# Kernel optimization log

Hardware: AMD Instinct MI355X
Metric: run time of the kernel (lower is better)

The kernel has to match this reference:

```python
import jax, jax.numpy as jnp
import numpy as np

# Norse LIFParameters defaults (method='super', alpha=100)
DT = 1e-3
TAU_SYN_INV = 200.0   # 1 / 5e-3
TAU_MEM_INV = 100.0   # 1 / 1e-2
V_TH = 1.0
V_LEAK = 0.0
V_RESET = 0.0
ALPHA = 100.0

@jax.custom_vjp
def superspike(x):
    return (x > 0).astype(x.dtype)

def _ss_fwd(x):
    return superspike(x), x

def _ss_bwd(x, g):
    return (g / (ALPHA * jnp.abs(x) + 1.0) ** 2,)

superspike.defvjp(_ss_fwd, _ss_bwd)

T, B, F, H1, OUT = 100, 512, 784, 1024, 10

def setup_inputs() -> dict:
    key = jax.random.key(0)
    k1, k2, k3 = jax.random.split(key, 3)
    x = jax.random.normal(k1, (T, B, F), jnp.float32)
    # fc0: Linear(784, h1) with bias
    W0 = jax.random.normal(k2, (H1, F), jnp.float32) / np.sqrt(F)
    b0 = jnp.zeros((H1,), jnp.float32)
    # LILinearCell input_weights: Linear(h1, 10) without bias
    Wout = jax.random.normal(k3, (OUT, H1), jnp.float32) / np.sqrt(H1)
    return {"x": x, "W0": W0, "b0": b0, "Wout": Wout}

def reference(x, W0, b0, Wout):
    Tn, Bn, Fn = x.shape
    H = W0.shape[0]
    O = Wout.shape[0]

    def step(state, xt):
        v_lif, i_lif, v_li, i_li = state
        z_in = xt @ W0.T + b0                                    # [B, H]
        # LIF cell step
        v_dec = v_lif + DT * TAU_MEM_INV * ((V_LEAK - v_lif) + i_lif)
        i_dec = i_lif * (1.0 - DT * TAU_SYN_INV)
        z = superspike(v_dec - V_TH)                             # spikes [B, H]
        v_new = (1.0 - z) * v_dec + z * V_RESET
        i_new = i_dec + z_in
        # LI linear cell step (voltage output)
        v_li_new = v_li + DT * TAU_MEM_INV * ((V_LEAK - v_li) + i_li)
        i_li_new = i_li * (1.0 - DT * TAU_SYN_INV) + z @ Wout.T  # [B, O]
        return (v_new, i_new, v_li_new, i_li_new), v_li_new

    z0 = lambda s: jnp.zeros(s, x.dtype)
    init = (z0((Bn, H)), z0((Bn, H)), z0((Bn, O)), z0((Bn, O)))
    _, voltages = jax.lax.scan(step, init, x)
    return voltages  # [T, B, 10]
```

## Files before the change

### kernel.cpp

```cpp
#include <hip/hip_runtime.h>

#define T_TOT 100
#define BATCH 512
#define FIN   784
#define HID   1024
#define NOUT  10
#define KP    800
#define BK    32
#define KSTEPS 25
#define NGRP  16

#define A_HI 0
#define A_LO 8192
#define B_HI 16384
#define B_LO 24576

typedef _Float16 f16x8 __attribute__((ext_vector_type(8)));
typedef float    f32x4 __attribute__((ext_vector_type(4)));

#define AS1C(p) ((const __attribute__((address_space(1))) void*)(p))
#define AS3(p)  ((__attribute__((address_space(3))) void*)(p))

__global__ __launch_bounds__(256)
void cvt_split(const float* __restrict__ src, _Float16* __restrict__ hi,
               _Float16* __restrict__ lo, int nrows)
{
    int idx = blockIdx.x * 256 + threadIdx.x;
    if (idx >= nrows * 100) return;
    int row = idx / 100;
    int k0  = (idx - row * 100) * 8;
    f16x8 h, l;
    if (k0 < FIN) {
        float4 a = *(const float4*)(src + (size_t)row * FIN + k0);
        float4 b = *(const float4*)(src + (size_t)row * FIN + k0 + 4);
        float xs[8] = {a.x, a.y, a.z, a.w, b.x, b.y, b.z, b.w};
        #pragma unroll
        for (int j = 0; j < 8; ++j) {
            _Float16 hh = (_Float16)xs[j];
            h[j] = hh;
            l[j] = (_Float16)((xs[j] - (float)hh) * 4096.0f);
        }
    } else {
        #pragma unroll
        for (int j = 0; j < 8; ++j) { h[j] = (_Float16)0.f; l[j] = (_Float16)0.f; }
    }
    *(f16x8*)(hi + (size_t)row * KP + k0) = h;
    *(f16x8*)(lo + (size_t)row * KP + k0) = l;
}

__global__ __launch_bounds__(256, 2)
void gemm_fused(const float* __restrict__ X,
                const _Float16* __restrict__ Whi, const _Float16* __restrict__ Wlo,
                const float* __restrict__ bias, float* __restrict__ Z, int mb)
{
    __shared__ char smem[65536];
    const int tid  = threadIdx.x;
    const int lane = tid & 63;
    const int wid  = tid >> 6;
    const int wm   = wid >> 1;
    const int wn   = wid & 1;
    const int fr   = lane & 15;
    const int fg   = lane >> 4;

    const int j = blockIdx.x;
    int bm, bn;
    if ((mb & 7) == 0) {
        bm = (j & 7) | ((j >> 6) << 3);
        bn = (j >> 3) & 7;
    } else {
        bm = j >> 3;
        bn = j & 7;
    }
    const size_t row0 = (size_t)bm * 128;
    const int    col0 = bn * 128;

    f32x4 accm[4][4], accc[4][4];
    #pragma unroll
    for (int a = 0; a < 4; ++a)
        #pragma unroll
        for (int b = 0; b < 4; ++b) {
            accm[a][b] = (f32x4){0.f, 0.f, 0.f, 0.f};
            accc[a][b] = (f32x4){0.f, 0.f, 0.f, 0.f};
        }

    const int arow  = tid >> 1;
    const int ahalf = tid & 1;
    float4 ar[4];
    auto aload = [&](int kt) {
        const int kof = kt * BK + ahalf * 16;
        const float* src = X + (row0 + arow) * (size_t)FIN + kof;
        #pragma unroll
        for (int c = 0; c < 4; ++c)
            ar[c] = (kof + c * 4 < FIN) ? *(const float4*)(src + c * 4)
                                        : make_float4(0.f, 0.f, 0.f, 0.f);
    };
    auto cvtwrite = [&](int buf) {
        char* base = smem + buf * 32768;
        #pragma unroll
        for (int cc = 0; cc < 2; ++cc) {
            float xs[8];
            *(float4*)&xs[0] = ar[cc * 2];
            *(float4*)&xs[4] = ar[cc * 2 + 1];
            f16x8 h, l;
            #pragma unroll
            for (int e = 0; e < 8; ++e) {
                _Float16 hh = (_Float16)xs[e];
                h[e] = hh;
                l[e] = (_Float16)((xs[e] - (float)hh) * 4096.0f);
            }
            const int ch  = ahalf * 2 + cc;
            const int chs = ch ^ ((arow >> 1) & 3);
            const int off = arow * 64 + chs * 16;
            *(f16x8*)(base + A_HI + off) = h;
            *(f16x8*)(base + A_LO + off) = l;
        }
    };
    auto stageB = [&](int buf, int kt) {
        const int kof = kt * BK;
        #pragma unroll
        for (int q = 0; q < 2; ++q) {
            const int lin = q * 256 + tid;
            const int row = lin >> 2;
            const int pos = lin & 3;
            const int gg  = pos ^ ((row >> 1) & 3);
            const int ldsw = buf * 32768 + q * 4096 + wid * 1024;
            const size_t gb = (size_t)(col0 + row) * KP + kof + gg * 8;
            __builtin_amdgcn_global_load_lds(AS1C(Whi + gb), AS3(smem + ldsw + B_HI), 16, 0, 0);
            __builtin_amdgcn_global_load_lds(AS1C(Wlo + gb), AS3(smem + ldsw + B_LO), 16, 0, 0);
        }
    };

    auto compute = [&](int buf) {
        const char* base = smem + buf * 32768;
        f16x8 ah[4], al[4], bh[4], bl[4];
        #pragma unroll
        for (int mf = 0; mf < 4; ++mf) {
            const int row = wm * 64 + mf * 16 + fr;
            const int off = row * 64 + ((fg ^ ((row >> 1) & 3)) << 4);
            ah[mf] = *(const f16x8*)(base + A_HI + off);
            al[mf] = *(const f16x8*)(base + A_LO + off);
        }
        #pragma unroll
        for (int nf = 0; nf < 4; ++nf) {
            const int row = wn * 64 + nf * 16 + fr;
            const int off = row * 64 + ((fg ^ ((row >> 1) & 3)) << 4);
            bh[nf] = *(const f16x8*)(base + B_HI + off);
            bl[nf] = *(const f16x8*)(base + B_LO + off);
        }
        #pragma unroll
        for (int mf = 0; mf < 4; ++mf)
            #pragma unroll
            for (int nf = 0; nf < 4; ++nf) {
                accm[mf][nf] = __builtin_amdgcn_mfma_f32_16x16x32_f16(ah[mf], bh[nf], accm[mf][nf], 0, 0, 0);
                accc[mf][nf] = __builtin_amdgcn_mfma_f32_16x16x32_f16(ah[mf], bl[nf], accc[mf][nf], 0, 0, 0);
                accc[mf][nf] = __builtin_amdgcn_mfma_f32_16x16x32_f16(al[mf], bh[nf], accc[mf][nf], 0, 0, 0);
            }
    };

    aload(0);
    stageB(0, 0);
    cvtwrite(0);

    int buf = 0;
    for (int kt = 0; kt < KSTEPS; ++kt) {
        __syncthreads();
        if (kt + 1 < KSTEPS) {
            aload(kt + 1);
            stageB(buf ^ 1, kt + 1);
        }
        compute(buf);
        if (kt + 1 < KSTEPS) cvtwrite(buf ^ 1);
        buf ^= 1;
    }

    #pragma unroll
    for (int nf = 0; nf < 4; ++nf) {
        const int colg = col0 + wn * 64 + nf * 16 + fr;
        const float bv = bias[colg];
        #pragma unroll
        for (int mf = 0; mf < 4; ++mf) {
            const size_t rowg = row0 + wm * 64 + mf * 16 + fg * 4;
            #pragma unroll
            for (int i = 0; i < 4; ++i)
                Z[(rowg + i) * HID + colg] =
                    accm[mf][nf][i] + accc[mf][nf][i] * 2.44140625e-4f + bv;
        }
    }
}

__device__ __forceinline__ float dpp_sum16(float v)
{
    int x;
    x = __builtin_amdgcn_update_dpp(0, __builtin_bit_cast(int, v), 0xB1, 0xF, 0xF, true);
    v += __builtin_bit_cast(float, x);
    x = __builtin_amdgcn_update_dpp(0, __builtin_bit_cast(int, v), 0x4E, 0xF, 0xF, true);
    v += __builtin_bit_cast(float, x);
    x = __builtin_amdgcn_update_dpp(0, __builtin_bit_cast(int, v), 0x141, 0xF, 0xF, true);
    v += __builtin_bit_cast(float, x);
    x = __builtin_amdgcn_update_dpp(0, __builtin_bit_cast(int, v), 0x140, 0xF, 0xF, true);
    v += __builtin_bit_cast(float, x);
    return v;
}

__global__ __launch_bounds__(256, 2)
void lif_scan(const float* __restrict__ Z, const float* __restrict__ Wout,
              float* __restrict__ S,
              float* __restrict__ st_v, float* __restrict__ st_i,
              int tn, int first, int last)
{
#pragma clang fp contract(off)
    const int tid   = threadIdx.x;
    const int b     = blockIdx.x;
    const int lane  = tid & 63;
    const int w     = tid >> 6;
    const int hglob = w * 256 + lane * 4;

    float wreg[NOUT][4];
    #pragma unroll
    for (int o = 0; o < NOUT; ++o) {
        float4 t4 = *(const float4*)&Wout[o * HID + hglob];
        wreg[o][0] = t4.x; wreg[o][1] = t4.y; wreg[o][2] = t4.z; wreg[o][3] = t4.w;
    }

    float v[4], cu[4];
    if (first) {
        #pragma unroll
        for (int jj = 0; jj < 4; ++jj) { v[jj] = 0.f; cu[jj] = 0.f; }
    } else {
        float4 tv = *(const float4*)&st_v[(size_t)b * HID + hglob];
        float4 ti = *(const float4*)&st_i[(size_t)b * HID + hglob];
        v[0]=tv.x; v[1]=tv.y; v[2]=tv.z; v[3]=tv.w;
        cu[0]=ti.x; cu[1]=ti.y; cu[2]=ti.z; cu[3]=ti.w;
    }

    const float*  Zb    = Z + (size_t)b * HID + hglob;
    const size_t  ZSTEP = (size_t)BATCH * HID;
    const int     g     = w * 4 + (lane >> 4);

    float4 ring[8];
    #pragma unroll
    for (int u = 0; u < 8; ++u)
        ring[u] = (u < tn) ? *(const float4*)(Zb + (size_t)u * ZSTEP)
                           : make_float4(0.f, 0.f, 0.f, 0.f);

    for (int tb = 0; tb < tn; tb += 8) {
        #pragma unroll
        for (int u = 0; u < 8; ++u) {
            const int t = tb + u;
            if (t >= tn) break;
            float4 zc = ring[u];
            if (t + 8 < tn)
                ring[u] = *(const float4*)(Zb + (size_t)(t + 8) * ZSTEP);

            const float za[4] = {zc.x, zc.y, zc.z, zc.w};
            float zf[4];
            bool anyz = false;
            #pragma unroll
            for (int jj = 0; jj < 4; ++jj) {
                float tmp  = (0.0f - v[jj]) + cu[jj];
                float vdec = v[jj] + 0.1f * tmp;
                bool  z    = vdec > 1.0f;
                zf[jj] = z ? 1.0f : 0.0f;
                anyz   = anyz || z;
                v[jj]  = z ? 0.0f : vdec;
                cu[jj] = cu[jj] * 0.8f + za[jj];
            }

            float p[NOUT];
            #pragma unroll
            for (int o = 0; o < NOUT; ++o) p[o] = 0.f;

            if (__any(anyz)) {
                if (anyz) {
                    #pragma unroll
                    for (int o = 0; o < NOUT; ++o)
                        p[o] = zf[0]*wreg[o][0] + zf[1]*wreg[o][1]
                             + zf[2]*wreg[o][2] + zf[3]*wreg[o][3];
                }
                #pragma unroll
                for (int o = 0; o < NOUT; ++o) p[o] = dpp_sum16(p[o]);
            }

            if ((lane & 15) == 0) {
                float* sp = S + ((size_t)t * BATCH + b) * (NGRP * NOUT) + g * NOUT;
                #pragma unroll
                for (int o = 0; o < NOUT; ++o) sp[o] = p[o];
            }
        }
    }

    if (!last) {
        *(float4*)&st_v[(size_t)b * HID + hglob] = make_float4(v[0], v[1], v[2], v[3]);
        *(float4*)&st_i[(size_t)b * HID + hglob] = make_float4(cu[0], cu[1], cu[2], cu[3]);
    }
}

__global__ __launch_bounds__(256)
void li_scan(const float* __restrict__ S, float* __restrict__ out,
             float* __restrict__ st_vli, float* __restrict__ st_ili,
             int t0, int tn, int first, int last)
{
#pragma clang fp contract(off)
    const int team = blockIdx.x * 16 + (threadIdx.x >> 4);
    const int g    = threadIdx.x & 15;
    const int b    = team / NOUT;
    const int o    = team - b * NOUT;

    float vli = 0.f, ili = 0.f;
    if (!first) { vli = st_vli[team]; ili = st_ili[team]; }

    const float* Sp   = S + ((size_t)b * NGRP + g) * NOUT + o;
    const size_t STEP = (size_t)BATCH * NGRP * NOUT;

    float rg[4];
    #pragma unroll
    for (int u = 0; u < 4; ++u)
        rg[u] = (u < tn) ? Sp[(size_t)u * STEP] : 0.f;

    for (int tb = 0; tb < tn; tb += 4) {
        #pragma unroll
        for (int u = 0; u < 4; ++u) {
            const int t = tb + u;
            if (t >= tn) break;
            float val = rg[u];
            if (t + 4 < tn) rg[u] = Sp[(size_t)(t + 4) * STEP];
            float s = dpp_sum16(val);
            float tmp  = (0.0f - vli) + ili;
            float vnew = vli + 0.1f * tmp;
            ili = ili * 0.8f + s;
            vli = vnew;
            if (g == 0)
                out[((size_t)(t0 + t) * BATCH + b) * NOUT + o] = vnew;
        }
    }
    if (!last && g == 0) { st_vli[team] = vli; st_ili[team] = ili; }
}

extern "C" void kernel_launch(void* const* d_in, const int* in_sizes, int n_in,
                              void* d_out, int out_size, void* d_ws, size_t ws_size,
                              hipStream_t stream)
{
    const float* x    = (const float*)d_in[0];
    const float* W0   = (const float*)d_in[1];
    const float* b0   = (const float*)d_in[2];
    const float* Wout = (const float*)d_in[3];
    float* out = (float*)d_out;

    char* ws = (char*)d_ws;
    float* st_v   = (float*)ws;
    float* st_i   = st_v   + (size_t)BATCH * HID;
    float* st_vli = st_i   + (size_t)BATCH * HID;
    float* st_ili = st_vli + BATCH * NOUT;
    _Float16* Whi = (_Float16*)(st_ili + BATCH * NOUT);
    _Float16* Wlo = Whi + (size_t)HID * KP;
    char* dyn = (char*)(Wlo + (size_t)HID * KP);

    const size_t fixed = (size_t)(dyn - ws);
    const size_t per_t = (size_t)BATCH * HID * 4
                       + (size_t)BATCH * NGRP * NOUT * 4;
    size_t avail = (ws_size > fixed) ? ws_size - fixed : 0;
    int tch = (int)(avail / per_t);
    if (tch > T_TOT) tch = T_TOT;
    if (tch >= 2) tch &= ~1;
    if (tch < 1) tch = 1;

    float* Zbuf = (float*)dyn;
    float* Sbuf = (float*)(dyn + (size_t)tch * BATCH * HID * 4);

    hipLaunchKernelGGL(cvt_split, dim3((HID * 100 + 255) / 256), dim3(256), 0, stream,
                       W0, Whi, Wlo, HID);

    for (int t0 = 0; t0 < T_TOT; t0 += tch) {
        const int tn    = (T_TOT - t0 < tch) ? (T_TOT - t0) : tch;
        const int nrows = tn * BATCH;
        const int mb    = nrows / 128;

        hipLaunchKernelGGL(gemm_fused, dim3(mb * 8), dim3(256), 0, stream,
                           x + (size_t)t0 * BATCH * FIN, Whi, Wlo, b0, Zbuf, mb);
        hipLaunchKernelGGL(lif_scan, dim3(BATCH), dim3(256), 0, stream,
                           Zbuf, Wout, Sbuf, st_v, st_i,
                           tn, (t0 == 0) ? 1 : 0, (t0 + tn >= T_TOT) ? 1 : 0);
        hipLaunchKernelGGL(li_scan, dim3((BATCH * NOUT) / 16), dim3(256), 0, stream,
                           Sbuf, out, st_vli, st_ili,
                           t0, tn, (t0 == 0) ? 1 : 0, (t0 + tn >= T_TOT) ? 1 : 0);
    }
}
```

Baseline: 450.3 us.

## Load A fragments directly into registers, bypassing LDS staging

Each wave now loads its own A rows straight from global memory in MFMA fragment layout and converts them to fp16 hi/lo in registers, so the A tile no longer goes through LDS. LDS shrinks to the double-buffered B tiles only, which could allow more blocks per CU and removes the A LDS writes and reads. In exchange, the two waves sharing the same rows (wn=0/1) each load the same A data redundantly from global memory. The per-lane 32-byte loads have a strided pattern that may coalesce poorly. The MFMA section is also wrapped in s_setprio.

```diff
diff --git a/kernel.cpp b/kernel.cpp
--- a/kernel.cpp
+++ b/kernel.cpp
@@ -10,10 +10,9 @@
 #define KSTEPS 25
 #define NGRP  16
 
-#define A_HI 0
-#define A_LO 8192
-#define B_HI 16384
-#define B_LO 24576
+#define B_HI 0
+#define B_LO 8192
+#define BBUF 16384
 
 typedef _Float16 f16x8 __attribute__((ext_vector_type(8)));
 typedef float    f32x4 __attribute__((ext_vector_type(4)));
@@ -53,7 +52,7 @@
                 const _Float16* __restrict__ Whi, const _Float16* __restrict__ Wlo,
                 const float* __restrict__ bias, float* __restrict__ Z, int mb)
 {
-    __shared__ char smem[65536];
+    __shared__ char smem[2 * BBUF];
     const int tid  = threadIdx.x;
     const int lane = tid & 63;
     const int wid  = tid >> 6;
@@ -83,24 +82,26 @@
             accc[a][b] = (f32x4){0.f, 0.f, 0.f, 0.f};
         }
 
-    const int arow  = tid >> 1;
-    const int ahalf = tid & 1;
-    float4 ar[4];
+    const float* Abase = X + (row0 + wm * 64 + fr) * (size_t)FIN;
+    float4 ar[4][2];
+    f16x8  ah[4], al[4];
+
     auto aload = [&](int kt) {
-        const int kof = kt * BK + ahalf * 16;
-        const float* src = X + (row0 + arow) * (size_t)FIN + kof;
-        #pragma unroll
-        for (int c = 0; c < 4; ++c)
-            ar[c] = (kof + c * 4 < FIN) ? *(const float4*)(src + c * 4)
-                                        : make_float4(0.f, 0.f, 0.f, 0.f);
+        const int k0 = kt * BK + fg * 8;
+        const bool ok = (k0 < FIN);
+        #pragma unroll
+        for (int mf = 0; mf < 4; ++mf) {
+            const float* src = Abase + (size_t)mf * 16 * FIN + k0;
+            ar[mf][0] = ok ? *(const float4*)(src)     : make_float4(0.f,0.f,0.f,0.f);
+            ar[mf][1] = ok ? *(const float4*)(src + 4) : make_float4(0.f,0.f,0.f,0.f);
+        }
     };
-    auto cvtwrite = [&](int buf) {
-        char* base = smem + buf * 32768;
-        #pragma unroll
-        for (int cc = 0; cc < 2; ++cc) {
+    auto acvt = [&]() {
+        #pragma unroll
+        for (int mf = 0; mf < 4; ++mf) {
             float xs[8];
-            *(float4*)&xs[0] = ar[cc * 2];
-            *(float4*)&xs[4] = ar[cc * 2 + 1];
+            *(float4*)&xs[0] = ar[mf][0];
+            *(float4*)&xs[4] = ar[mf][1];
             f16x8 h, l;
             #pragma unroll
             for (int e = 0; e < 8; ++e) {
@@ -108,13 +109,11 @@
                 h[e] = hh;
                 l[e] = (_Float16)((xs[e] - (float)hh) * 4096.0f);
             }
-            const int ch  = ahalf * 2 + cc;
-            const int chs = ch ^ ((arow >> 1) & 3);
-            const int off = arow * 64 + chs * 16;
-            *(f16x8*)(base + A_HI + off) = h;
-            *(f16x8*)(base + A_LO + off) = l;
+            ah[mf] = h;
+            al[mf] = l;
         }
     };
+
     auto stageB = [&](int buf, int kt) {
         const int kof = kt * BK;
         #pragma unroll
@@ -123,23 +122,27 @@
             const int row = lin >> 2;
             const int pos = lin & 3;
             const int gg  = pos ^ ((row >> 1) & 3);
-            const int ldsw = buf * 32768 + q * 4096 + wid * 1024;
+            const int ldsw = buf * BBUF + q * 4096 + wid * 1024;
             const size_t gb = (size_t)(col0 + row) * KP + kof + gg * 8;
             __builtin_amdgcn_global_load_lds(AS1C(Whi + gb), AS3(smem + ldsw + B_HI), 16, 0, 0);
             __builtin_amdgcn_global_load_lds(AS1C(Wlo + gb), AS3(smem + ldsw + B_LO), 16, 0, 0);
         }
     };
 
-    auto compute = [&](int buf) {
-        const char* base = smem + buf * 32768;
-        f16x8 ah[4], al[4], bh[4], bl[4];
-        #pragma unroll
-        for (int mf = 0; mf < 4; ++mf) {
-            const int row = wm * 64 + mf * 16 + fr;
-            const int off = row * 64 + ((fg ^ ((row >> 1) & 3)) << 4);
-            ah[mf] = *(const f16x8*)(base + A_HI + off);
-            al[mf] = *(const f16x8*)(base + A_LO + off);
-        }
+    aload(0);
+    stageB(0, 0);
+    acvt();
+
+    int buf = 0;
+    for (int kt = 0; kt < KSTEPS; ++kt) {
+        __syncthreads();
+        if (kt + 1 < KSTEPS) {
+            stageB(buf ^ 1, kt + 1);
+            aload(kt + 1);
+        }
+
+        const char* base = smem + buf * BBUF;
+        f16x8 bh[4], bl[4];
         #pragma unroll
         for (int nf = 0; nf < 4; ++nf) {
             const int row = wn * 64 + nf * 16 + fr;
@@ -147,6 +150,8 @@
             bh[nf] = *(const f16x8*)(base + B_HI + off);
             bl[nf] = *(const f16x8*)(base + B_LO + off);
         }
+
+        __builtin_amdgcn_s_setprio(1);
         #pragma unroll
         for (int mf = 0; mf < 4; ++mf)
             #pragma unroll
@@ -155,21 +160,9 @@
                 accc[mf][nf] = __builtin_amdgcn_mfma_f32_16x16x32_f16(ah[mf], bl[nf], accc[mf][nf], 0, 0, 0);
                 accc[mf][nf] = __builtin_amdgcn_mfma_f32_16x16x32_f16(al[mf], bh[nf], accc[mf][nf], 0, 0, 0);
             }
-    };
-
-    aload(0);
-    stageB(0, 0);
-    cvtwrite(0);
-
-    int buf = 0;
-    for (int kt = 0; kt < KSTEPS; ++kt) {
-        __syncthreads();
-        if (kt + 1 < KSTEPS) {
-            aload(kt + 1);
-            stageB(buf ^ 1, kt + 1);
-        }
-        compute(buf);
-        if (kt + 1 < KSTEPS) cvtwrite(buf ^ 1);
+        __builtin_amdgcn_s_setprio(0);
+
+        if (kt + 1 < KSTEPS) acvt();
         buf ^= 1;
     }
 
```

New measurement: 504.9 us. 12.1% more time.
